# Kernel tuning notes

Measured on AMD Instinct MI355X. Metric: run time of the kernel, lower is better.

Reference implementation:

```python
import jax, jax.numpy as jnp
import numpy as np

N_NODES = 8   # chain DAG 0->1->...->7
B = 2048      # n_samples
T_STEPS = 8   # end_wind
Z_DIM = 32    # latent_dim // 2
EMB = 8       # emb_dim
GRU_H = 24
HID = 64


def setup_inputs() -> dict:
    key = jax.random.key(0)
    ks = jax.random.split(key, 20)
    def rn(k, shape, scale=0.1):
        return jax.random.normal(k, shape, jnp.float32) * scale
    return {
        "z": jax.random.normal(ks[0], (N_NODES, B, T_STEPS, Z_DIM), jnp.float32),
        "cond_w1": rn(ks[1], (N_NODES, 32, 1)),
        "cond_b1": rn(ks[2], (N_NODES, 32)),
        "cond_w2": rn(ks[3], (N_NODES, EMB, 32)),
        "cond_b2": rn(ks[4], (N_NODES, EMB)),
        "proj_w": rn(ks[5], (N_NODES, GRU_H, Z_DIM + 2 * EMB)),  # node 0 uses first 40 cols
        "proj_b": rn(ks[6], (N_NODES, GRU_H)),
        "gru_proj_w": rn(ks[7], (GRU_H, GRU_H)),
        "gru_proj_b": rn(ks[8], (GRU_H,)),
        "gru_wih": rn(ks[9], (N_NODES, 2, 3 * GRU_H, GRU_H)),
        "gru_whh": rn(ks[10], (N_NODES, 2, 3 * GRU_H, GRU_H)),
        "gru_bih": rn(ks[11], (N_NODES, 2, 3 * GRU_H)),
        "gru_bhh": rn(ks[12], (N_NODES, 2, 3 * GRU_H)),
        "cm_w1": rn(ks[13], (N_NODES, HID, GRU_H)),
        "cm_b1": rn(ks[14], (N_NODES, HID)),
        "cm_w2": rn(ks[15], (N_NODES, HID, HID)),
        "cm_b2": rn(ks[16], (N_NODES, HID)),
        "cm_w3": rn(ks[17], (N_NODES, 1, HID)),
        "cm_b3": rn(ks[18], (N_NODES, 1)),
        "end_wind": T_STEPS,
    }


def _leaky(x):
    return jnp.where(x >= 0, x, 0.01 * x)  # nn.LeakyReLU default slope


def _gru_layer(x, wih, whh, bih, bhh):
    """torch nn.GRU single layer, batch_first. x: [B, L, H] -> [B, L, H]."""
    h0 = jnp.zeros((x.shape[0], GRU_H), x.dtype)
    def step(h, xt):
        gi = xt @ wih.T + bih            # [B, 3H], gate order r, z, n
        gh = h @ whh.T + bhh
        i_r, i_z, i_n = jnp.split(gi, 3, axis=-1)
        h_r, h_z, h_n = jnp.split(gh, 3, axis=-1)
        r = jax.nn.sigmoid(i_r + h_r)
        zg = jax.nn.sigmoid(i_z + h_z)
        n = jnp.tanh(i_n + r * h_n)
        hn = (1.0 - zg) * n + zg * h
        return hn, hn
    _, ys = jax.lax.scan(step, h0, jnp.swapaxes(x, 0, 1))
    return jnp.swapaxes(ys, 0, 1)


def _forward(z, cond_w1, cond_b1, cond_w2, cond_b2, proj_w, proj_b,
             gru_proj_w, gru_proj_b, gru_wih, gru_whh, gru_bih, gru_bhh,
             cm_w1, cm_b1, cm_w2, cm_b2, cm_w3, cm_b3, end_wind):
    n_nodes, bsz = z.shape[0], z.shape[1]
    dt = z.dtype

    def cond_net(n, x):  # x: [B, L, 1] -> [B, L, EMB]
        h = jax.nn.relu(x @ cond_w1[n].T + cond_b1[n])
        return h @ cond_w2[n].T + cond_b2[n]

    def pipeline(n, z_mod):  # decode_pipeline: proj -> leaky -> gru_proj -> 2-layer GRU -> CausalMap
        w = proj_w[n][:, : z_mod.shape[-1]]
        h = _leaky(z_mod @ w.T + proj_b[n])
        g = h @ gru_proj_w.T + gru_proj_b
        y = _gru_layer(g, gru_wih[n, 0], gru_whh[n, 0], gru_bih[n, 0], gru_bhh[n, 0])
        y = _gru_layer(y, gru_wih[n, 1], gru_whh[n, 1], gru_bih[n, 1], gru_bhh[n, 1])
        d = jax.nn.relu(y @ cm_w1[n].T + cm_b1[n])
        d = jax.nn.relu(d @ cm_w2[n].T + cm_b2[n])
        return d @ cm_w3[n].T + cm_b3[n]  # [B, L, 1]

    decoded = [None] * n_nodes
    reals = [[] for _ in range(n_nodes)]
    for idx in range(end_wind):
        # chain DAG: in-degree grouping (deg 0 = node 0, deg 1 = nodes 1..7 in order)
        # coincides with node order 0..N-1.
        for node in range(n_nodes):
            z_mod = z[node][:, : idx + 1]                       # [B, idx+1, Z_DIM]
            if idx != 0:
                emb_self = cond_net(node, decoded[node])        # [B, idx, EMB]
                emb_self = jnp.concatenate(
                    [emb_self, jnp.zeros((bsz, 1, EMB), dt)], axis=1)
            else:
                emb_self = jnp.zeros((bsz, 1, EMB), dt)
            z_mod = jnp.concatenate([z_mod, emb_self], axis=2)
            if node > 0:  # single predecessor node-1, already decoded this idx
                if idx != 0:
                    emb_p = cond_net(node - 1, decoded[node - 1])  # [B, idx+1, EMB]
                else:
                    emb_p = jnp.zeros((bsz, 1, EMB), dt)
                z_mod = jnp.concatenate([z_mod, emb_p], axis=2)
            d = pipeline(node, z_mod)                           # [B, idx+1, 1]
            decoded[node] = d
            reals[node].append(d[:, idx:idx + 1, 0])
    # [B, T, N]
    return jnp.stack([jnp.concatenate(r, axis=1) for r in reals], axis=-1)


def reference(z, cond_w1, cond_b1, cond_w2, cond_b2, proj_w, proj_b,
              gru_proj_w, gru_proj_b, gru_wih, gru_whh, gru_bih, gru_bhh,
              cm_w1, cm_b1, cm_w2, cm_b2, cm_w3, cm_b3, end_wind):
    return _forward(z, cond_w1, cond_b1, cond_w2, cond_b2, proj_w, proj_b,
                    gru_proj_w, gru_proj_b, gru_wih, gru_whh, gru_bih, gru_bhh,
                    cm_w1, cm_b1, cm_w2, cm_b2, cm_w3, cm_b3, int(end_wind))
```

## Files before the change

kernel.cpp:

```cpp
#include <hip/hip_runtime.h>


#define NT 64

__device__ __forceinline__ float sigm(float x) { return 1.0f / (1.0f + __expf(-x)); }
__device__ __forceinline__ float tanh_fast(float x) {
  x = fminf(15.0f, fmaxf(-15.0f, x));
  float e = __expf(2.0f * x);
  return (e - 1.0f) / (e + 1.0f);
}
__device__ __forceinline__ float leaky(float x) { return x >= 0.0f ? x : 0.01f * x; }

template <int N4>
__device__ __forceinline__ float dotv2(const float* __restrict__ w, const float* h) {
  const float4* w4 = reinterpret_cast<const float4*>(w);
  const float4* h4 = reinterpret_cast<const float4*>(h);
  float a0 = 0.0f, a1 = 0.0f;
#pragma unroll
  for (int i = 0; i < N4; i += 2) {
    float4 x0 = w4[i], y0 = h4[i];
    float4 x1 = w4[i + 1], y1 = h4[i + 1];
    a0 = fmaf(x0.x, y0.x, a0); a0 = fmaf(x0.y, y0.y, a0);
    a0 = fmaf(x0.z, y0.z, a0); a0 = fmaf(x0.w, y0.w, a0);
    a1 = fmaf(x1.x, y1.x, a1); a1 = fmaf(x1.y, y1.y, a1);
    a1 = fmaf(x1.z, y1.z, a1); a1 = fmaf(x1.w, y1.w, a1);
  }
  return a0 + a1;
}

template <int N4>
__device__ __forceinline__ float dotv4(const float* __restrict__ w, const float* h) {
  const float4* w4 = reinterpret_cast<const float4*>(w);
  const float4* h4 = reinterpret_cast<const float4*>(h);
  float a0 = 0.0f, a1 = 0.0f, a2 = 0.0f, a3 = 0.0f;
#pragma unroll
  for (int i = 0; i < N4; i += 4) {
    float4 x0 = w4[i], y0 = h4[i];
    float4 x1 = w4[i + 1], y1 = h4[i + 1];
    float4 x2 = w4[i + 2], y2 = h4[i + 2];
    float4 x3 = w4[i + 3], y3 = h4[i + 3];
    a0 = fmaf(x0.x, y0.x, a0); a0 = fmaf(x0.y, y0.y, a0);
    a0 = fmaf(x0.z, y0.z, a0); a0 = fmaf(x0.w, y0.w, a0);
    a1 = fmaf(x1.x, y1.x, a1); a1 = fmaf(x1.y, y1.y, a1);
    a1 = fmaf(x1.z, y1.z, a1); a1 = fmaf(x1.w, y1.w, a1);
    a2 = fmaf(x2.x, y2.x, a2); a2 = fmaf(x2.y, y2.y, a2);
    a2 = fmaf(x2.z, y2.z, a2); a2 = fmaf(x2.w, y2.w, a2);
    a3 = fmaf(x3.x, y3.x, a3); a3 = fmaf(x3.y, y3.y, a3);
    a3 = fmaf(x3.z, y3.z, a3); a3 = fmaf(x3.w, y3.w, a3);
  }
  return (a0 + a1) + (a2 + a3);
}

__device__ __forceinline__ void gates_stage(
    const float* __restrict__ wih, const float* __restrict__ bih,
    const float* srcp, float* s_gi, int L, int lane, int rowB) {
  float4 WA[6], WB[6];
  const float4* wa = reinterpret_cast<const float4*>(wih + (size_t)lane * 24);
  const float4* wb = reinterpret_cast<const float4*>(wih + (size_t)rowB * 24);
#pragma unroll
  for (int i = 0; i < 6; ++i) { WA[i] = wa[i]; WB[i] = wb[i]; }
  const float bA = bih[lane], bB = bih[rowB];
  int t = 0;
#pragma unroll 1
  for (; t + 1 < L; t += 2) {
    const float4* h0 = reinterpret_cast<const float4*>(srcp + t * 24);
    const float4* h1 = reinterpret_cast<const float4*>(srcp + t * 24 + 24);
    float a0 = bA, a1 = bA, c0 = bB, c1 = bB;
#pragma unroll
    for (int i = 0; i < 6; ++i) {
      float4 p = h0[i], q = h1[i], A = WA[i], Bv = WB[i];
      a0 = fmaf(A.x, p.x, a0); a0 = fmaf(A.y, p.y, a0);
      a0 = fmaf(A.z, p.z, a0); a0 = fmaf(A.w, p.w, a0);
      a1 = fmaf(A.x, q.x, a1); a1 = fmaf(A.y, q.y, a1);
      a1 = fmaf(A.z, q.z, a1); a1 = fmaf(A.w, q.w, a1);
      c0 = fmaf(Bv.x, p.x, c0); c0 = fmaf(Bv.y, p.y, c0);
      c0 = fmaf(Bv.z, p.z, c0); c0 = fmaf(Bv.w, p.w, c0);
      c1 = fmaf(Bv.x, q.x, c1); c1 = fmaf(Bv.y, q.y, c1);
      c1 = fmaf(Bv.z, q.z, c1); c1 = fmaf(Bv.w, q.w, c1);
    }
    s_gi[t * 72 + lane] = a0;
    s_gi[t * 72 + 72 + lane] = a1;
    if (lane < 8) {
      s_gi[t * 72 + 64 + lane] = c0;
      s_gi[t * 72 + 136 + lane] = c1;
    }
  }
  if (t < L) {
    const float4* h0 = reinterpret_cast<const float4*>(srcp + t * 24);
    float a0 = bA, c0 = bB;
#pragma unroll
    for (int i = 0; i < 6; ++i) {
      float4 p = h0[i], A = WA[i], Bv = WB[i];
      a0 = fmaf(A.x, p.x, a0); a0 = fmaf(A.y, p.y, a0);
      a0 = fmaf(A.z, p.z, a0); a0 = fmaf(A.w, p.w, a0);
      c0 = fmaf(Bv.x, p.x, c0); c0 = fmaf(Bv.y, p.y, c0);
      c0 = fmaf(Bv.z, p.z, c0); c0 = fmaf(Bv.w, p.w, c0);
    }
    s_gi[t * 72 + lane] = a0;
    if (lane < 8) s_gi[t * 72 + 64 + lane] = c0;
  }
}

__device__ __forceinline__ void rec_stage(
    const float* __restrict__ whh, const float* __restrict__ bhh,
    const float* s_gi, float* s_hid, float* s_y, int L, int lane, int jq, int half) {
  float4 Wr[3], Wz[3], Wn[3];
  const float4* wr = reinterpret_cast<const float4*>(whh + jq * 24 + half * 12);
  const float4* wz = reinterpret_cast<const float4*>(whh + (24 + jq) * 24 + half * 12);
  const float4* wn = reinterpret_cast<const float4*>(whh + (48 + jq) * 24 + half * 12);
#pragma unroll
  for (int i = 0; i < 3; ++i) { Wr[i] = wr[i]; Wz[i] = wz[i]; Wn[i] = wn[i]; }
  const float bR = half ? 0.0f : bhh[jq];
  const float bZ = half ? 0.0f : bhh[24 + jq];
  const float bN = half ? 0.0f : bhh[48 + jq];
  if (lane < 24) s_hid[lane] = 0.0f;
  int cur = 0;
#pragma unroll 1
  for (int t = 0; t < L; ++t) {
    const float4* hp = reinterpret_cast<const float4*>(s_hid + cur * 24 + half * 12);
    float gr = bR, gz = bZ, gn = bN;
#pragma unroll
    for (int i = 0; i < 3; ++i) {
      float4 hh = hp[i];
      gr = fmaf(Wr[i].x, hh.x, gr); gr = fmaf(Wr[i].y, hh.y, gr);
      gr = fmaf(Wr[i].z, hh.z, gr); gr = fmaf(Wr[i].w, hh.w, gr);
      gz = fmaf(Wz[i].x, hh.x, gz); gz = fmaf(Wz[i].y, hh.y, gz);
      gz = fmaf(Wz[i].z, hh.z, gz); gz = fmaf(Wz[i].w, hh.w, gz);
      gn = fmaf(Wn[i].x, hh.x, gn); gn = fmaf(Wn[i].y, hh.y, gn);
      gn = fmaf(Wn[i].z, hh.z, gn); gn = fmaf(Wn[i].w, hh.w, gn);
    }
    gr += __shfl_xor(gr, 32);
    gz += __shfl_xor(gz, 32);
    gn += __shfl_xor(gn, 32);
    const float* gi = s_gi + t * 72;
    float r   = sigm(gi[jq] + gr);
    float zg  = sigm(gi[24 + jq] + gz);
    float nn2 = tanh_fast(gi[48 + jq] + r * gn);
    float hold = s_hid[cur * 24 + jq];
    float hnew = fmaf(zg, hold - nn2, nn2);
    if (lane < 24) {
      s_hid[(cur ^ 1) * 24 + lane] = hnew;
      s_y[t * 24 + lane] = hnew;
    }
    cur ^= 1;
  }
}

__global__ __launch_bounds__(NT, 2) void tcm_kernel(
    const float* __restrict__ z,
    const float* __restrict__ cond_w1, const float* __restrict__ cond_b1,
    const float* __restrict__ cond_w2, const float* __restrict__ cond_b2,
    const float* __restrict__ proj_w, const float* __restrict__ proj_b,
    const float* __restrict__ gpw, const float* __restrict__ gpb,
    const float* __restrict__ gru_wih, const float* __restrict__ gru_whh,
    const float* __restrict__ gru_bih, const float* __restrict__ gru_bhh,
    const float* __restrict__ cm_w1, const float* __restrict__ cm_b1,
    const float* __restrict__ cm_w2, const float* __restrict__ cm_b2,
    const float* __restrict__ cm_w3, const float* __restrict__ cm_b3,
    const int* __restrict__ endw,
    float* __restrict__ out, int Btot) {
  __shared__ __align__(16) float lds[3488];
  float* s_x   = lds;
  float* s_h   = lds + 384;
  float* s_g   = lds + 576;
  float* s_gi  = lds + 768;
  float* s_y   = lds + 1344;
  float* s_hid = lds + 1536;
  float* s_d1  = lds + 1584;
  float* s_d2  = lds + 2128;
  float* s_dd  = lds + 2672;
  float* s_ch  = lds + 2688;
  float* s_emb = lds + 2976;

  const int lane = threadIdx.x;
  const int b = blockIdx.x;
  const int T = endw[0];
  const int jm = lane & 31;
  const int half = lane >> 5;
  const int jq = jm < 24 ? jm : 0;
  const int rowB = 64 + (lane & 7);

#pragma unroll 1
  for (int idx = 0; idx < T; ++idx) {
    const int L = idx + 1;
#pragma unroll 1
    for (int n = 0; n < 8; ++n) {
      const float* wih0 = gru_wih + (size_t)(n * 2) * 1728;
      const float* wih1 = wih0 + 1728;
      const float* whh0 = gru_whh + (size_t)(n * 2) * 1728;
      const float* whh1 = whh0 + 1728;
      const float* bih0 = gru_bih + (n * 2) * 72;
      const float* bih1 = bih0 + 72;
      const float* bhh0 = gru_bhh + (n * 2) * 72;
      const float* bhh1 = bhh0 + 72;

      if (lane < L * 8) {
        const float4* z4 = reinterpret_cast<const float4*>(
            z + ((size_t)n * Btot + b) * 8 * 32);
        int t = lane >> 3, q = lane & 7;
        reinterpret_cast<float4*>(s_x)[t * 12 + q] = z4[t * 8 + q];
      }
#pragma unroll 1
      for (int it = lane; it < L * 16; it += NT) {
        int t = it >> 4, c = it & 15;
        float v = 0.0f;
        if (c < 8) {
          if (t < idx) v = s_emb[n * 64 + t * 8 + c];
        } else {
          if (n > 0 && idx > 0) v = s_emb[(n - 1) * 64 + t * 8 + (c - 8)];
        }
        s_x[t * 48 + 32 + c] = v;
      }
      __syncthreads();
#pragma unroll 1
      for (int it = lane; it < L * 24; it += NT) {
        int t = it / 24, j = it - t * 24;
        float acc = proj_b[n * 24 + j] +
                    dotv2<12>(proj_w + (size_t)(n * 24 + j) * 48, s_x + t * 48);
        s_h[t * 24 + j] = leaky(acc);
      }
      __syncthreads();
#pragma unroll 1
      for (int it = lane; it < L * 24; it += NT) {
        int t = it / 24, j = it - t * 24;
        s_g[t * 24 + j] = gpb[j] + dotv2<6>(gpw + j * 24, s_h + t * 24);
      }
      __syncthreads();
      gates_stage(wih0, bih0, s_g, s_gi, L, lane, rowB);
      __syncthreads();
      rec_stage(whh0, bhh0, s_gi, s_hid, s_y, L, lane, jq, half);
      __syncthreads();
      gates_stage(wih1, bih1, s_y, s_gi, L, lane, rowB);
      __syncthreads();
      rec_stage(whh1, bhh1, s_gi, s_hid, s_y, L, lane, jq, half);
      __syncthreads();
      {
        float4 C1[6];
        const float4* p = reinterpret_cast<const float4*>(
            cm_w1 + (size_t)(n * 64 + lane) * 24);
#pragma unroll
        for (int i = 0; i < 6; ++i) C1[i] = p[i];
        const float bb = cm_b1[n * 64 + lane];
        int t = 0;
#pragma unroll 1
        for (; t + 1 < L; t += 2) {
          const float4* y0 = reinterpret_cast<const float4*>(s_y + t * 24);
          const float4* y1 = reinterpret_cast<const float4*>(s_y + t * 24 + 24);
          float a0 = bb, a1 = bb;
#pragma unroll
          for (int i = 0; i < 6; ++i) {
            float4 pp = y0[i], q = y1[i], W = C1[i];
            a0 = fmaf(W.x, pp.x, a0); a0 = fmaf(W.y, pp.y, a0);
            a0 = fmaf(W.z, pp.z, a0); a0 = fmaf(W.w, pp.w, a0);
            a1 = fmaf(W.x, q.x, a1); a1 = fmaf(W.y, q.y, a1);
            a1 = fmaf(W.z, q.z, a1); a1 = fmaf(W.w, q.w, a1);
          }
          s_d1[t * 68 + lane] = fmaxf(a0, 0.0f);
          s_d1[t * 68 + 68 + lane] = fmaxf(a1, 0.0f);
        }
        if (t < L) {
          float acc = bb;
          const float4* y0 = reinterpret_cast<const float4*>(s_y + t * 24);
#pragma unroll
          for (int i = 0; i < 6; ++i) {
            float4 pp = y0[i], W = C1[i];
            acc = fmaf(W.x, pp.x, acc); acc = fmaf(W.y, pp.y, acc);
            acc = fmaf(W.z, pp.z, acc); acc = fmaf(W.w, pp.w, acc);
          }
          s_d1[t * 68 + lane] = fmaxf(acc, 0.0f);
        }
      }
      __syncthreads();
      {
        float4 C2[16];
        const float4* p = reinterpret_cast<const float4*>(
            cm_w2 + (size_t)(n * 64 + lane) * 64);
#pragma unroll
        for (int i = 0; i < 16; ++i) C2[i] = p[i];
        const float bb = cm_b2[n * 64 + lane];
        int t = 0;
#pragma unroll 1
        for (; t + 1 < L; t += 2) {
          const float4* d0 = reinterpret_cast<const float4*>(s_d1 + t * 68);
          const float4* d1 = reinterpret_cast<const float4*>(s_d1 + t * 68 + 68);
          float a0 = bb, a1 = 0.0f, c0 = bb, c1 = 0.0f;
#pragma unroll
          for (int i = 0; i < 16; i += 2) {
            float4 W0 = C2[i], W1 = C2[i + 1];
            float4 p0 = d0[i], p1 = d0[i + 1], q0 = d1[i], q1 = d1[i + 1];
            a0 = fmaf(W0.x, p0.x, a0); a0 = fmaf(W0.y, p0.y, a0);
            a0 = fmaf(W0.z, p0.z, a0); a0 = fmaf(W0.w, p0.w, a0);
            a1 = fmaf(W1.x, p1.x, a1); a1 = fmaf(W1.y, p1.y, a1);
            a1 = fmaf(W1.z, p1.z, a1); a1 = fmaf(W1.w, p1.w, a1);
            c0 = fmaf(W0.x, q0.x, c0); c0 = fmaf(W0.y, q0.y, c0);
            c0 = fmaf(W0.z, q0.z, c0); c0 = fmaf(W0.w, q0.w, c0);
            c1 = fmaf(W1.x, q1.x, c1); c1 = fmaf(W1.y, q1.y, c1);
            c1 = fmaf(W1.z, q1.z, c1); c1 = fmaf(W1.w, q1.w, c1);
          }
          s_d2[t * 68 + lane] = fmaxf(a0 + a1, 0.0f);
          s_d2[t * 68 + 68 + lane] = fmaxf(c0 + c1, 0.0f);
        }
        if (t < L) {
          const float4* d0 = reinterpret_cast<const float4*>(s_d1 + t * 68);
          float a0 = bb, a1 = 0.0f;
#pragma unroll
          for (int i = 0; i < 16; i += 2) {
            float4 W0 = C2[i], W1 = C2[i + 1];
            float4 p0 = d0[i], p1 = d0[i + 1];
            a0 = fmaf(W0.x, p0.x, a0); a0 = fmaf(W0.y, p0.y, a0);
            a0 = fmaf(W0.z, p0.z, a0); a0 = fmaf(W0.w, p0.w, a0);
            a1 = fmaf(W1.x, p1.x, a1); a1 = fmaf(W1.y, p1.y, a1);
            a1 = fmaf(W1.z, p1.z, a1); a1 = fmaf(W1.w, p1.w, a1);
          }
          s_d2[t * 68 + lane] = fmaxf(a0 + a1, 0.0f);
        }
      }
      __syncthreads();
      if (lane < L) {
        int t = lane;
        float dv = cm_b3[n] + dotv4<16>(cm_w3 + n * 64, s_d2 + t * 68);
        s_dd[t] = dv;
        if (t == idx)
          out[((size_t)b * T + idx) * 8 + n] = dv;
      }
      __syncthreads();
#pragma unroll 1
      for (int it = lane; it < L * 32; it += NT) {
        int t = it >> 5, k = it & 31;
        s_ch[t * 36 + k] =
            fmaxf(fmaf(s_dd[t], cond_w1[n * 32 + k], cond_b1[n * 32 + k]), 0.0f);
      }
      __syncthreads();
      if (lane < L * 8) {
        int t = lane >> 3, c = lane & 7;
        s_emb[n * 64 + t * 8 + c] =
            cond_b2[n * 8 + c] +
            dotv2<8>(cond_w2 + (size_t)(n * 8 + c) * 32, s_ch + t * 36);
      }
      __syncthreads();
    }
  }
}

extern "C" void kernel_launch(void* const* d_in, const int* in_sizes, int n_in,
                              void* d_out, int out_size, void* d_ws, size_t ws_size,
                              hipStream_t stream) {
  const float* z       = (const float*)d_in[0];
  const float* cond_w1 = (const float*)d_in[1];
  const float* cond_b1 = (const float*)d_in[2];
  const float* cond_w2 = (const float*)d_in[3];
  const float* cond_b2 = (const float*)d_in[4];
  const float* proj_w  = (const float*)d_in[5];
  const float* proj_b  = (const float*)d_in[6];
  const float* gpw     = (const float*)d_in[7];
  const float* gpb     = (const float*)d_in[8];
  const float* gru_wih = (const float*)d_in[9];
  const float* gru_whh = (const float*)d_in[10];
  const float* gru_bih = (const float*)d_in[11];
  const float* gru_bhh = (const float*)d_in[12];
  const float* cm_w1   = (const float*)d_in[13];
  const float* cm_b1   = (const float*)d_in[14];
  const float* cm_w2   = (const float*)d_in[15];
  const float* cm_b2   = (const float*)d_in[16];
  const float* cm_w3   = (const float*)d_in[17];
  const float* cm_b3   = (const float*)d_in[18];
  const int*   endw    = (const int*)d_in[19];
  float* out = (float*)d_out;

  int Btot = in_sizes[0] / (8 * 8 * 32);

  tcm_kernel<<<Btot, NT, 0, stream>>>(
      z, cond_w1, cond_b1, cond_w2, cond_b2, proj_w, proj_b, gpw, gpb,
      gru_wih, gru_whh, gru_bih, gru_bhh, cm_w1, cm_b1, cm_w2, cm_b2,
      cm_w3, cm_b3, endw, out, Btot);
}
```

Before: 1.062 ms.

## Prefetch next-stage weights into registers and replace block barriers with LDS waitcnt

Hoists the global loads of each stage's weights (GRU input and hidden weights, MLP layers 1 and 2) so they are issued before the preceding stage's compute, overlapping load latency with work. It also swaps __syncthreads for a bare lgkmcnt wait, which is valid only because the block is a single 64-lane wavefront. Register pressure rises from holding two stages' weights at once, which may lower occupancy. One FMA order in dotv4 is also swapped.

```diff
diff --git a/kernel.cpp b/kernel.cpp
--- a/kernel.cpp
+++ b/kernel.cpp
@@ -2,6 +2,7 @@
 
 
 #define NT 64
+#define SYNC() asm volatile("s_waitcnt lgkmcnt(0)" ::: "memory")
 
 __device__ __forceinline__ float sigm(float x) { return 1.0f / (1.0f + __expf(-x)); }
 __device__ __forceinline__ float tanh_fast(float x) {
@@ -46,20 +47,38 @@
     a2 = fmaf(x2.x, y2.x, a2); a2 = fmaf(x2.y, y2.y, a2);
     a2 = fmaf(x2.z, y2.z, a2); a2 = fmaf(x2.w, y2.w, a2);
     a3 = fmaf(x3.x, y3.x, a3); a3 = fmaf(x3.y, y3.y, a3);
-    a3 = fmaf(x3.z, y3.z, a3); a3 = fmaf(x3.w, y3.w, a3);
+    a3 = fmaf(x3.w, y3.w, a3); a3 = fmaf(x3.z, y3.z, a3);
   }
   return (a0 + a1) + (a2 + a3);
 }
 
-__device__ __forceinline__ void gates_stage(
+__device__ __forceinline__ void load_gates_w(
     const float* __restrict__ wih, const float* __restrict__ bih,
-    const float* srcp, float* s_gi, int L, int lane, int rowB) {
-  float4 WA[6], WB[6];
+    int lane, int rowB, float4 WA[6], float4 WB[6], float& bA, float& bB) {
   const float4* wa = reinterpret_cast<const float4*>(wih + (size_t)lane * 24);
   const float4* wb = reinterpret_cast<const float4*>(wih + (size_t)rowB * 24);
 #pragma unroll
   for (int i = 0; i < 6; ++i) { WA[i] = wa[i]; WB[i] = wb[i]; }
-  const float bA = bih[lane], bB = bih[rowB];
+  bA = bih[lane]; bB = bih[rowB];
+}
+
+__device__ __forceinline__ void load_rec_w(
+    const float* __restrict__ whh, const float* __restrict__ bhh,
+    int jq, int half, float4 Wr[3], float4 Wz[3], float4 Wn[3],
+    float& bR, float& bZ, float& bN) {
+  const float4* wr = reinterpret_cast<const float4*>(whh + jq * 24 + half * 12);
+  const float4* wz = reinterpret_cast<const float4*>(whh + (24 + jq) * 24 + half * 12);
+  const float4* wn = reinterpret_cast<const float4*>(whh + (48 + jq) * 24 + half * 12);
+#pragma unroll
+  for (int i = 0; i < 3; ++i) { Wr[i] = wr[i]; Wz[i] = wz[i]; Wn[i] = wn[i]; }
+  bR = half ? 0.0f : bhh[jq];
+  bZ = half ? 0.0f : bhh[24 + jq];
+  bN = half ? 0.0f : bhh[48 + jq];
+}
+
+__device__ __forceinline__ void gates_comp(
+    const float4 WA[6], const float4 WB[6], float bA, float bB,
+    const float* srcp, float* s_gi, int L, int lane) {
   int t = 0;
 #pragma unroll 1
   for (; t + 1 < L; t += 2) {
@@ -101,18 +120,10 @@
   }
 }
 
-__device__ __forceinline__ void rec_stage(
-    const float* __restrict__ whh, const float* __restrict__ bhh,
+__device__ __forceinline__ void rec_comp(
+    const float4 Wr[3], const float4 Wz[3], const float4 Wn[3],
+    float bR, float bZ, float bN,
     const float* s_gi, float* s_hid, float* s_y, int L, int lane, int jq, int half) {
-  float4 Wr[3], Wz[3], Wn[3];
-  const float4* wr = reinterpret_cast<const float4*>(whh + jq * 24 + half * 12);
-  const float4* wz = reinterpret_cast<const float4*>(whh + (24 + jq) * 24 + half * 12);
-  const float4* wn = reinterpret_cast<const float4*>(whh + (48 + jq) * 24 + half * 12);
-#pragma unroll
-  for (int i = 0; i < 3; ++i) { Wr[i] = wr[i]; Wz[i] = wz[i]; Wn[i] = wn[i]; }
-  const float bR = half ? 0.0f : bhh[jq];
-  const float bZ = half ? 0.0f : bhh[24 + jq];
-  const float bN = half ? 0.0f : bhh[48 + jq];
   if (lane < 24) s_hid[lane] = 0.0f;
   int cur = 0;
 #pragma unroll 1
@@ -194,6 +205,9 @@
       const float* bhh0 = gru_bhh + (n * 2) * 72;
       const float* bhh1 = bhh0 + 72;
 
+      float4 WA[6], WB[6]; float bA, bB;
+      load_gates_w(wih0, bih0, lane, rowB, WA, WB, bA, bB);
+
       if (lane < L * 8) {
         const float4* z4 = reinterpret_cast<const float4*>(
             z + ((size_t)n * Btot + b) * 8 * 32);
@@ -211,7 +225,7 @@
         }
         s_x[t * 48 + 32 + c] = v;
       }
-      __syncthreads();
+      SYNC();
 #pragma unroll 1
       for (int it = lane; it < L * 24; it += NT) {
         int t = it / 24, j = it - t * 24;
@@ -219,34 +233,50 @@
                     dotv2<12>(proj_w + (size_t)(n * 24 + j) * 48, s_x + t * 48);
         s_h[t * 24 + j] = leaky(acc);
       }
-      __syncthreads();
+      SYNC();
 #pragma unroll 1
       for (int it = lane; it < L * 24; it += NT) {
         int t = it / 24, j = it - t * 24;
         s_g[t * 24 + j] = gpb[j] + dotv2<6>(gpw + j * 24, s_h + t * 24);
       }
-      __syncthreads();
-      gates_stage(wih0, bih0, s_g, s_gi, L, lane, rowB);
-      __syncthreads();
-      rec_stage(whh0, bhh0, s_gi, s_hid, s_y, L, lane, jq, half);
-      __syncthreads();
-      gates_stage(wih1, bih1, s_y, s_gi, L, lane, rowB);
-      __syncthreads();
-      rec_stage(whh1, bhh1, s_gi, s_hid, s_y, L, lane, jq, half);
-      __syncthreads();
+      SYNC();
+      float4 Wr[3], Wz[3], Wn[3]; float bR, bZ, bN;
+      load_rec_w(whh0, bhh0, jq, half, Wr, Wz, Wn, bR, bZ, bN);
+      gates_comp(WA, WB, bA, bB, s_g, s_gi, L, lane);
+      SYNC();
+      float4 WA1[6], WB1[6]; float bA1, bB1;
+      load_gates_w(wih1, bih1, lane, rowB, WA1, WB1, bA1, bB1);
+      rec_comp(Wr, Wz, Wn, bR, bZ, bN, s_gi, s_hid, s_y, L, lane, jq, half);
+      SYNC();
+      float4 Wr1[3], Wz1[3], Wn1[3]; float bR1, bZ1, bN1;
+      load_rec_w(whh1, bhh1, jq, half, Wr1, Wz1, Wn1, bR1, bZ1, bN1);
+      gates_comp(WA1, WB1, bA1, bB1, s_y, s_gi, L, lane);
+      SYNC();
+      float4 C1[6];
       {
-        float4 C1[6];
         const float4* p = reinterpret_cast<const float4*>(
             cm_w1 + (size_t)(n * 64 + lane) * 24);
 #pragma unroll
         for (int i = 0; i < 6; ++i) C1[i] = p[i];
-        const float bb = cm_b1[n * 64 + lane];
+      }
+      const float c1b = cm_b1[n * 64 + lane];
+      rec_comp(Wr1, Wz1, Wn1, bR1, bZ1, bN1, s_gi, s_hid, s_y, L, lane, jq, half);
+      SYNC();
+      float4 C2[16];
+      {
+        const float4* p = reinterpret_cast<const float4*>(
+            cm_w2 + (size_t)(n * 64 + lane) * 64);
+#pragma unroll
+        for (int i = 0; i < 16; ++i) C2[i] = p[i];
+      }
+      const float c2b = cm_b2[n * 64 + lane];
+      {
         int t = 0;
 #pragma unroll 1
         for (; t + 1 < L; t += 2) {
           const float4* y0 = reinterpret_cast<const float4*>(s_y + t * 24);
           const float4* y1 = reinterpret_cast<const float4*>(s_y + t * 24 + 24);
-          float a0 = bb, a1 = bb;
+          float a0 = c1b, a1 = c1b;
 #pragma unroll
           for (int i = 0; i < 6; ++i) {
             float4 pp = y0[i], q = y1[i], W = C1[i];
@@ -259,7 +289,7 @@
           s_d1[t * 68 + 68 + lane] = fmaxf(a1, 0.0f);
         }
         if (t < L) {
-          float acc = bb;
+          float acc = c1b;
           const float4* y0 = reinterpret_cast<const float4*>(s_y + t * 24);
 #pragma unroll
           for (int i = 0; i < 6; ++i) {
@@ -270,20 +300,14 @@
           s_d1[t * 68 + lane] = fmaxf(acc, 0.0f);
         }
       }
-      __syncthreads();
+      SYNC();
       {
-        float4 C2[16];
-        const float4* p = reinterpret_cast<const float4*>(
-            cm_w2 + (size_t)(n * 64 + lane) * 64);
-#pragma unroll
-        for (int i = 0; i < 16; ++i) C2[i] = p[i];
-        const float bb = cm_b2[n * 64 + lane];
         int t = 0;
 #pragma unroll 1
         for (; t + 1 < L; t += 2) {
           const float4* d0 = reinterpret_cast<const float4*>(s_d1 + t * 68);
           const float4* d1 = reinterpret_cast<const float4*>(s_d1 + t * 68 + 68);
-          float a0 = bb, a1 = 0.0f, c0 = bb, c1 = 0.0f;
+          float a0 = c2b, a1 = 0.0f, c0 = c2b, c1 = 0.0f;
 #pragma unroll
           for (int i = 0; i < 16; i += 2) {
             float4 W0 = C2[i], W1 = C2[i + 1];
@@ -302,7 +326,7 @@
         }
         if (t < L) {
           const float4* d0 = reinterpret_cast<const float4*>(s_d1 + t * 68);
-          float a0 = bb, a1 = 0.0f;
+          float a0 = c2b, a1 = 0.0f;
 #pragma unroll
           for (int i = 0; i < 16; i += 2) {
             float4 W0 = C2[i], W1 = C2[i + 1];
@@ -315,7 +339,7 @@
           s_d2[t * 68 + lane] = fmaxf(a0 + a1, 0.0f);
         }
       }
-      __syncthreads();
+      SYNC();
       if (lane < L) {
         int t = lane;
         float dv = cm_b3[n] + dotv4<16>(cm_w3 + n * 64, s_d2 + t * 68);
@@ -323,21 +347,21 @@
         if (t == idx)
           out[((size_t)b * T + idx) * 8 + n] = dv;
       }
-      __syncthreads();
+      SYNC();
 #pragma unroll 1
       for (int it = lane; it < L * 32; it += NT) {
         int t = it >> 5, k = it & 31;
         s_ch[t * 36 + k] =
             fmaxf(fmaf(s_dd[t], cond_w1[n * 32 + k], cond_b1[n * 32 + k]), 0.0f);
       }
-      __syncthreads();
+      SYNC();
       if (lane < L * 8) {
         int t = lane >> 3, c = lane & 7;
         s_emb[n * 64 + t * 8 + c] =
             cond_b2[n * 8 + c] +
             dotv2<8>(cond_w2 + (size_t)(n * 8 + c) * 32, s_ch + t * 36);
       }
-      __syncthreads();
+      SYNC();
     }
   }
 }
```

Measured after the change: 1.026 ms, median of 3. -3.4%, faster.
